# Optimization experiments

Hardware: AMD Instinct MI355X
Metric: run time of the kernel (lower is better)

## Reference

```python
import jax, jax.numpy as jnp
import numpy as np

B, T, Rn, D, O, E, H, C, TM = 20, 20, 20, 4096, 16, 512, 8, 68, 1900


def l2norm(x, axis=-1, eps=1e-12):
    return x / jnp.maximum(jnp.linalg.norm(x, axis=axis, keepdims=True), eps)


def setup_inputs() -> dict:
    key = jax.random.key(0)
    ks = jax.random.split(key, 10)
    return {
        "features": jax.random.normal(ks[0], (B, T, Rn, D), jnp.float32),
        "labels": jax.random.randint(ks[1], (B, O), 0, C),
        "temporal_mem": jax.random.normal(ks[2], (TM, T, D), jnp.float32),
        "entity_W": jax.random.normal(ks[3], (C, E), jnp.float32) / np.float32(np.sqrt(C)),
        "entity_b": jnp.zeros((E,), jnp.float32),
        "Wq": jax.random.normal(ks[4], (E, E), jnp.float32) / np.float32(np.sqrt(E)),
        "Wk": jax.random.normal(ks[5], (D, E), jnp.float32) / np.float32(np.sqrt(D)),
        "Wv": jax.random.normal(ks[6], (D, E), jnp.float32) / np.float32(np.sqrt(D)),
        "Wo": jax.random.normal(ks[7], (E, E), jnp.float32) / np.float32(np.sqrt(E)),
        "obj_W1": jax.random.normal(ks[8], (D, E), jnp.float32) / np.float32(np.sqrt(D)),
        "obj_b1": jnp.zeros((E,), jnp.float32),
        "obj_W2": jax.random.normal(ks[9], (E, 1), jnp.float32) / np.float32(np.sqrt(E)),
        "obj_b2": jnp.zeros((1,), jnp.float32),
    }


def reference(features, labels, temporal_mem, entity_W, entity_b, Wq, Wk, Wv, Wo,
              obj_W1, obj_b1, obj_W2, obj_b2):
    beta = 0.5   # loss mixing weight (module's beta)
    qgce = 0.7   # generalized-CE exponent
    Dh = E // H
    # region features, L2-normalized (dataset_feat == 'CVPR' path)
    Rf = l2norm(features)                                   # [B,T,Rn,D]

    # ---- temporal memory-bank kNN retrieval ----
    R_max = l2norm(jnp.max(Rf, axis=2))                     # [B,T,D] max-pool over regions
    mem_max = l2norm(jnp.max(temporal_mem, axis=1))         # [TM,D] max-pool over frames
    sim = jnp.einsum('btd,md->btm', R_max, mem_max)         # [B,T,TM]
    idx = jnp.argmax(sim, axis=-1)                          # [B,T] nearest memory slot
    Rp = temporal_mem[idx]                                  # [B,T,T,D] gathered memory videos
    mem_feat = jnp.max(Rp, axis=2)                          # [B,T,D]

    # ---- entity (object-label) embedding: one-hot with class 0 zeroed ----
    onehot = jax.nn.one_hot(labels, C, dtype=features.dtype)
    onehot = onehot * (labels != 0)[..., None].astype(features.dtype)
    Qe = onehot @ entity_W + entity_b                       # [B,O,E]

    # ---- multi-head attention fusion over regions + retrieved memory ----
    kv = jnp.concatenate([Rf.reshape(B, T * Rn, D), mem_feat], axis=1)  # [B,N,D]
    q = (Qe @ Wq).reshape(B, O, H, Dh)
    k = (kv @ Wk).reshape(B, -1, H, Dh)
    v = (kv @ Wv).reshape(B, -1, H, Dh)
    scores = jnp.einsum('bohd,bnhd->bhon', q, k) / np.float32(np.sqrt(Dh))
    attn = jax.nn.softmax(scores, axis=-1)
    fused = jnp.einsum('bhon,bnhd->bohd', attn, v).reshape(B, O, E) @ Wo  # [B,O,E]

    # ---- top-k region objectness selection + generalized CE ----
    QR = jax.lax.stop_gradient(jnp.mean(scores, axis=1)[:, :, :T * Rn].reshape(B, O, T, Rn))
    hi = jnp.argmax(QR, axis=-1)                            # [B,O,T] top-1 region
    lo = jnp.argmin(QR, axis=-1)                            # [B,O,T] low region
    bidx = jnp.arange(B)[:, None, None]
    tidx = jnp.arange(T)[None, None, :]
    R_high = Rf[bidx, tidx, hi]                             # [B,O,T,D]
    R_low = Rf[bidx, tidx, lo]                              # [B,O,T,D]
    osel = (labels != 0).astype(features.dtype)             # [B,O]
    onum = jnp.maximum(jnp.sum(osel, axis=1), 1.0)
    mlp = lambda x: jax.nn.sigmoid(jnp.tanh(x @ obj_W1 + obj_b1) @ obj_W2 + obj_b2)
    s_hi = mlp(R_high * osel[..., None, None]).squeeze(-1)  # [B,O,T]
    s_lo = mlp(R_low * osel[..., None, None]).squeeze(-1)
    gce_hi = jnp.mean((1.0 - (s_hi + 1e-7) ** qgce) / qgce * osel[..., None], axis=-1)
    gce_lo = jnp.mean((1.0 - (1.0 - s_lo + 1e-7) ** qgce) / qgce * osel[..., None], axis=-1)
    gce = jnp.mean(jnp.sum(gce_hi, axis=1) / onum) + jnp.mean(jnp.sum(gce_lo, axis=1) / onum)

    return fused + beta * gce
```

## Files before the change

### kernel.cpp

```cpp
#include <hip/hip_runtime.h>

#define B_   20
#define T_   20
#define RN   20
#define D_   4096
#define O_   16
#define E_   512
#define H_   8
#define DH   64
#define TM_  1900
#define NKV  420
#define MROWS (B_*NKV)
#define MPAD 8448
#define NW   1536
#define NSIM 1920
#define MSIM 512
#define CAP  256
#define SIMK 8

using f32x4  = __attribute__((ext_vector_type(4))) float;
using bf16x8 = __attribute__((ext_vector_type(8))) __bf16;

__device__ __forceinline__ unsigned short f2bf(float f){
  unsigned u = __float_as_uint(f);
  u += 0x7fffu + ((u >> 16) & 1u);
  return (unsigned short)(u >> 16);
}

__device__ __forceinline__ void st_bf4(unsigned short* dst, float4 v){
  ushort4 o = make_ushort4(f2bf(v.x), f2bf(v.y), f2bf(v.z), f2bf(v.w));
  *(ushort4*)dst = o;
}

__device__ __forceinline__ float bsum256(float v, float* sh){
  int t = threadIdx.x;
  for (int o = 32; o; o >>= 1) v += __shfl_down(v, o, 64);
  __syncthreads();
  if ((t & 63) == 0) sh[t >> 6] = v;
  __syncthreads();
  return sh[0] + sh[1] + sh[2] + sh[3];
}

__device__ __forceinline__ float bmax256(float v, float* sh){
  int t = threadIdx.x;
  for (int o = 32; o; o >>= 1) v = fmaxf(v, __shfl_down(v, o, 64));
  __syncthreads();
  if ((t & 63) == 0) sh[t >> 6] = v;
  __syncthreads();
  return fmaxf(fmaxf(sh[0], sh[1]), fmaxf(sh[2], sh[3]));
}

__device__ __forceinline__ void gld16(const void* g, void* l){
  __builtin_amdgcn_global_load_lds(
      (const __attribute__((address_space(1))) unsigned int*)g,
      (__attribute__((address_space(3))) unsigned int*)l, 16, 0, 0);
}

__global__ __launch_bounds__(256) void k_pre(
    const float* __restrict__ F, const float* __restrict__ TMm,
    const float* __restrict__ Wk, const float* __restrict__ Wv, const float* __restrict__ W1,
    unsigned short* __restrict__ Wall,
    unsigned short* __restrict__ A, float* __restrict__ rmaxr, float* __restrict__ rmsum,
    unsigned short* __restrict__ ubf,
    float* __restrict__ umax, float* __restrict__ msum, unsigned short* __restrict__ wnorm,
    const int* __restrict__ labels, const float* __restrict__ entW, const float* __restrict__ entB,
    const float* __restrict__ Wq, float* __restrict__ q){
  __shared__ char smem[4352];
  int bid = blockIdx.x, t = threadIdx.x;
  if (bid < 1920){
    int m = bid;
    if (m >= TM_){
      int4 zz = make_int4(0,0,0,0);
      int4* row = (int4*)(wnorm + (size_t)m*D_);
      row[t] = zz; row[t + 256] = zz;
      return;
    }
    float* sh = (float*)smem;
    const float* base = TMm + (size_t)m*T_*D_;
    float4 mx[4];
#pragma unroll
    for (int i = 0; i < 4; ++i) mx[i] = make_float4(-1e30f,-1e30f,-1e30f,-1e30f);
    for (int f = 0; f < T_; ++f){
#pragma unroll
      for (int i = 0; i < 4; ++i){
        float4 v = *(const float4*)(base + (size_t)f*D_ + i*1024 + t*4);
        mx[i].x = fmaxf(mx[i].x, v.x); mx[i].y = fmaxf(mx[i].y, v.y);
        mx[i].z = fmaxf(mx[i].z, v.z); mx[i].w = fmaxf(mx[i].w, v.w);
      }
    }
    float s = 0.f;
#pragma unroll
    for (int i = 0; i < 4; ++i){
      *(float4*)(umax + (size_t)m*D_ + i*1024 + t*4) = mx[i];
      s += mx[i].x*mx[i].x + mx[i].y*mx[i].y + mx[i].z*mx[i].z + mx[i].w*mx[i].w;
    }
    s = bsum256(s, sh);
    if (t == 0) msum[m] = s;
    float inv = 1.f / fmaxf(sqrtf(s), 1e-12f);
#pragma unroll
    for (int i = 0; i < 4; ++i){
      float4 u = mx[i];
      u.x *= inv; u.y *= inv; u.z *= inv; u.w *= inv;
      st_bf4(wnorm + (size_t)m*D_ + i*1024 + t*4, u);
    }
  } else if (bid < 2432){
    int bt = bid - 1920;
    if (bt >= 400){
      int4 zz = make_int4(0,0,0,0);
      int4* row = (int4*)(ubf + (size_t)bt*D_);
      row[t] = zz; row[t + 256] = zz;
      return;
    }
    float* sh = (float*)smem;
    int b = bt / T_, tt = bt % T_;
    const float* fb = F + (size_t)bt*RN*D_;
    unsigned short* ab = A + ((size_t)b*NKV + (size_t)tt*RN)*D_;
    float4 mx[4];
#pragma unroll
    for (int i = 0; i < 4; ++i) mx[i] = make_float4(-1e30f,-1e30f,-1e30f,-1e30f);
    for (int r = 0; r < RN; ++r){
      float4 v[4];
      float s = 0.f;
#pragma unroll
      for (int i = 0; i < 4; ++i){
        v[i] = *(const float4*)(fb + (size_t)r*D_ + i*1024 + t*4);
        s += v[i].x*v[i].x + v[i].y*v[i].y + v[i].z*v[i].z + v[i].w*v[i].w;
      }
      s = bsum256(s, sh);
      float ri = 1.f / fmaxf(sqrtf(s), 1e-12f);
#pragma unroll
      for (int i = 0; i < 4; ++i){
        v[i].x *= ri; v[i].y *= ri; v[i].z *= ri; v[i].w *= ri;
        st_bf4(ab + (size_t)r*D_ + i*1024 + t*4, v[i]);
        mx[i].x = fmaxf(mx[i].x, v[i].x); mx[i].y = fmaxf(mx[i].y, v[i].y);
        mx[i].z = fmaxf(mx[i].z, v[i].z); mx[i].w = fmaxf(mx[i].w, v[i].w);
      }
    }
    float s2 = 0.f;
#pragma unroll
    for (int i = 0; i < 4; ++i){
      *(float4*)(rmaxr + (size_t)bt*D_ + i*1024 + t*4) = mx[i];
      s2 += mx[i].x*mx[i].x + mx[i].y*mx[i].y + mx[i].z*mx[i].z + mx[i].w*mx[i].w;
    }
    s2 = bsum256(s2, sh);
    if (t == 0) rmsum[bt] = s2;
    float inv = 1.f / fmaxf(sqrtf(s2), 1e-12f);
#pragma unroll
    for (int i = 0; i < 4; ++i){
      float4 u = mx[i];
      u.x *= inv; u.y *= inv; u.z *= inv; u.w *= inv;
      st_bf4(ubf + (size_t)bt*D_ + i*1024 + t*4, u);
    }
  } else if (bid < 8576){
    int wti = bid - 2432;
    float* tile = (float*)smem;
    int kb = (wti & 127) * 32, nb = (wti >> 7) * 32;
    const float* src; int nc0;
    if (nb < 512)      { src = Wk; nc0 = nb; }
    else if (nb < 1024){ src = Wv; nc0 = nb - 512; }
    else               { src = W1; nc0 = nb - 1024; }
    int tx = t & 31, ty = t >> 5;
#pragma unroll
    for (int j = 0; j < 4; ++j){
      int k = kb + ty + j*8;
      tile[(ty + j*8)*33 + tx] = src[(size_t)k*E_ + nc0 + tx];
    }
    __syncthreads();
#pragma unroll
    for (int j = 0; j < 4; ++j){
      int n = nb + ty + j*8;
      int k = kb + tx;
      Wall[(size_t)n*D_ + k] = f2bf(tile[tx*33 + ty + j*8]);
    }
  } else {
    int bo = bid - 8576;
    float* qe = (float*)smem;
    int lab = labels[bo];
    float sel = (lab != 0) ? 1.f : 0.f;
    qe[t]       = sel * entW[(size_t)lab*E_ + t]       + entB[t];
    qe[t + 256] = sel * entW[(size_t)lab*E_ + t + 256] + entB[t + 256];
    __syncthreads();
    float a0 = 0.f, a1 = 0.f;
    for (int ep = 0; ep < E_; ++ep){
      float r = qe[ep];
      a0 += r * Wq[(size_t)ep*E_ + t];
      a1 += r * Wq[(size_t)ep*E_ + t + 256];
    }
    q[(size_t)bo*E_ + t] = a0;
    q[(size_t)bo*E_ + t + 256] = a1;
  }
}

__global__ __launch_bounds__(256, 2) void k_gemm(const unsigned short* __restrict__ A,
                                                 const unsigned short* __restrict__ Bw,
                                                 float* __restrict__ C,
                                                 int nNt, int ldc, int doswz, int nwg,
                                                 int nblk, int nkt, size_t cpart){
  __shared__ char lds[32768];
  int part = blockIdx.x / nblk;
  int bid  = blockIdx.x % nblk;
  if (doswz){ int q = nwg >> 3; bid = (bid & 7)*q + (bid >> 3); }
  int mt = bid / nNt, nt = bid % nNt;
  int tid = threadIdx.x, wv = tid >> 6, l = tid & 63;
  int wr = (wv >> 1) * 64, wc = (wv & 1) * 64;
  const char* Ab = (const char*)A + (size_t)mt*128*(size_t)(D_*2);
  const char* Bb = (const char*)Bw + (size_t)nt*128*(size_t)(D_*2);
  C += (size_t)part * cpart;
  f32x4 acc[4][4];
#pragma unroll
  for (int m = 0; m < 4; ++m)
#pragma unroll
    for (int n = 0; n < 4; ++n) acc[m][n] = (f32x4){0.f,0.f,0.f,0.f};
  int kt0 = part * nkt;
  for (int kt = kt0; kt < kt0 + nkt; ++kt){
    int ktoff = kt*128;
#pragma unroll
    for (int i = 0; i < 4; ++i){
      int idx = i*256 + tid;
      int row = idx >> 3, u = idx & 7;
      int ul = u ^ (row & 7);
      gld16(Ab + (size_t)row*(D_*2) + ktoff + ul*16, lds + i*4096 + wv*1024);
      gld16(Bb + (size_t)row*(D_*2) + ktoff + ul*16, lds + 16384 + i*4096 + wv*1024);
    }
    __syncthreads();
#pragma unroll
    for (int kk = 0; kk < 2; ++kk){
      bf16x8 av[4], bv[4];
#pragma unroll
      for (int m = 0; m < 4; ++m){
        int row = wr + m*16 + (l & 15);
        int u = (kk*4 + (l >> 4)) ^ (row & 7);
        av[m] = *(const bf16x8*)(lds + row*128 + u*16);
      }
#pragma unroll
      for (int n = 0; n < 4; ++n){
        int row = wc + n*16 + (l & 15);
        int u = (kk*4 + (l >> 4)) ^ (row & 7);
        bv[n] = *(const bf16x8*)(lds + 16384 + row*128 + u*16);
      }
#pragma unroll
      for (int m = 0; m < 4; ++m)
#pragma unroll
        for (int n = 0; n < 4; ++n)
          acc[m][n] = __builtin_amdgcn_mfma_f32_16x16x32_bf16(av[m], bv[n], acc[m][n], 0, 0, 0);
    }
    __syncthreads();
  }
  int rq = (l >> 4) * 4, cq = l & 15;
  size_t crow0 = (size_t)mt*128 + wr, ccol0 = (size_t)nt*128 + wc;
#pragma unroll
  for (int m = 0; m < 4; ++m)
#pragma unroll
    for (int n = 0; n < 4; ++n){
      size_t r0 = crow0 + m*16 + rq, c0 = ccol0 + n*16 + cq;
#pragma unroll
      for (int j = 0; j < 4; ++j)
        C[(r0 + j)*ldc + c0] = acc[m][n][j];
    }
}

__global__ __launch_bounds__(512, 1) void k_gemm256(const unsigned short* __restrict__ A,
                                                    const unsigned short* __restrict__ Bw,
                                                    float* __restrict__ C,
                                                    int nNt, int ldc, int nwg){
  __shared__ char lds[131072];
  int bid = blockIdx.x;
  {
    int q8 = nwg >> 3, r8 = nwg & 7, x = bid & 7, s = bid >> 3;
    bid = (x < r8 ? x*(q8+1) : r8*(q8+1) + (x-r8)*q8) + s;
  }
  int mt = bid / nNt, nt = bid % nNt;
  int tid = threadIdx.x, wid = tid >> 6, l = tid & 63;
  int wr = (wid >> 2) * 128;
  int wc = (wid & 3) * 64;
  int fr = l & 15, fq = l >> 4;
  const char* Ab = (const char*)A + (size_t)mt*256*(size_t)(D_*2);
  const char* Bb = (const char*)Bw + (size_t)nt*256*(size_t)(D_*2);
  f32x4 acc[8][4];
#pragma unroll
  for (int m = 0; m < 8; ++m)
#pragma unroll
    for (int n = 0; n < 4; ++n) acc[m][n] = (f32x4){0.f,0.f,0.f,0.f};

#pragma unroll
  for (int i = 0; i < 4; ++i){
    int idx = i*512 + tid;
    int row = idx >> 3, u = idx & 7;
    int ul = u ^ (row & 7);
    gld16(Ab + (size_t)row*(D_*2) + (size_t)(ul*16), lds + idx*16);
    gld16(Bb + (size_t)row*(D_*2) + (size_t)(ul*16), lds + 32768 + idx*16);
  }
  __syncthreads();

  int c = 0;
  for (int kt = 0; kt < D_/64; ++kt){
    if (kt < D_/64 - 1){
      int ktoff = (kt + 1) * 128;
      char* dA = lds + (c^1)*65536;
      char* dB = dA + 32768;
#pragma unroll
      for (int i = 0; i < 4; ++i){
        int idx = i*512 + tid;
        int row = idx >> 3, u = idx & 7;
        int ul = u ^ (row & 7);
        gld16(Ab + (size_t)row*(D_*2) + ktoff + ul*16, dA + idx*16);
        gld16(Bb + (size_t)row*(D_*2) + ktoff + ul*16, dB + idx*16);
      }
    }
    const char* LA = lds + c*65536;
    const char* LB = LA + 32768;
    bf16x8 bv[4][2];
#pragma unroll
    for (int n = 0; n < 4; ++n)
#pragma unroll
      for (int kk = 0; kk < 2; ++kk){
        int row = wc + n*16 + fr;
        int u = (kk*4 + fq) ^ (row & 7);
        bv[n][kk] = *(const bf16x8*)(LB + row*128 + u*16);
      }
    __builtin_amdgcn_s_setprio(1);
#pragma unroll
    for (int mp = 0; mp < 4; ++mp){
      bf16x8 av[2][2];
#pragma unroll
      for (int mm = 0; mm < 2; ++mm)
#pragma unroll
        for (int kk = 0; kk < 2; ++kk){
          int row = wr + (mp*2 + mm)*16 + fr;
          int u = (kk*4 + fq) ^ (row & 7);
          av[mm][kk] = *(const bf16x8*)(LA + row*128 + u*16);
        }
#pragma unroll
      for (int mm = 0; mm < 2; ++mm)
#pragma unroll
        for (int n = 0; n < 4; ++n)
#pragma unroll
          for (int kk = 0; kk < 2; ++kk)
            acc[mp*2 + mm][n] = __builtin_amdgcn_mfma_f32_16x16x32_bf16(
                av[mm][kk], bv[n][kk], acc[mp*2 + mm][n], 0, 0, 0);
    }
    __builtin_amdgcn_s_setprio(0);
    __syncthreads();
    c ^= 1;
  }
  size_t crow0 = (size_t)mt*256 + wr, ccol0 = (size_t)nt*256 + wc;
#pragma unroll
  for (int m = 0; m < 8; ++m)
#pragma unroll
    for (int n = 0; n < 4; ++n){
      size_t r0 = crow0 + m*16 + fq*4, c0 = ccol0 + n*16 + fr;
#pragma unroll
      for (int j = 0; j < 4; ++j)
        C[(r0 + j)*ldc + c0] = acc[m][n][j];
    }
}

__global__ __launch_bounds__(256) void k_pick(const float* __restrict__ simp,
                                              const float* __restrict__ rmaxr, const float* __restrict__ rmsum,
                                              const float* __restrict__ umax, const float* __restrict__ msum,
                                              unsigned short* __restrict__ A){
  int bt = blockIdx.x, t = threadIdx.x;
  if (bt >= 400){
    int4 z = make_int4(0,0,0,0);
    int4* row = (int4*)(A + (size_t)(MROWS + bt - 400)*D_);
    row[t] = z; row[t + 256] = z;
    return;
  }
  __shared__ float srow[NSIM];
  __shared__ float sh[4];
  __shared__ int cnt;
  __shared__ int cl[CAP];
  for (int m = t; m < NSIM; m += 256){
    float s = 0.f;
#pragma unroll
    for (int p = 0; p < SIMK; ++p)
      s += simp[(size_t)p*MSIM*NSIM + (size_t)bt*NSIM + m];
    srow[m] = s;
  }
  if (t == 0) cnt = 0;
  __syncthreads();
  float mx = -1e30f;
  for (int m = t; m < TM_; m += 256) mx = fmaxf(mx, srow[m]);
  mx = bmax256(mx, sh);
  float thr = mx - 2.5e-4f;
  for (int m = t; m < TM_; m += 256){
    if (srow[m] >= thr){
      int p = atomicAdd(&cnt, 1);
      if (p < CAP) cl[p] = m;
    }
  }
  __syncthreads();
  int cn = cnt < CAP ? cnt : CAP;
  float rinvv = 1.f / fmaxf(sqrtf(rmsum[bt]), 1e-12f);
  const float* a = rmaxr + (size_t)bt*D_;
  float best = -1e30f; int bestm = 0x7fffffff;
  for (int ci = 0; ci < cn; ++ci){
    int m = cl[ci];
    const float* wrow = umax + (size_t)m*D_;
    float p = 0.f;
    for (int i = t*4; i < D_; i += 1024){
      float4 av = *(const float4*)(a + i);
      float4 wv = *(const float4*)(wrow + i);
      p += av.x*wv.x + av.y*wv.y + av.z*wv.z + av.w*wv.w;
    }
    p = bsum256(p, sh);
    float sim = p * rinvv * (1.f / fmaxf(sqrtf(msum[m]), 1e-12f));
    if (sim > best || (sim == best && m < bestm)){ best = sim; bestm = m; }
  }
  int b = bt / T_, tt = bt % T_;
  unsigned short* dst = A + ((size_t)b*NKV + 400 + tt)*D_;
  const float* src = umax + (size_t)bestm*D_;
#pragma unroll
  for (int i = 0; i < 4; ++i){
    size_t off = (size_t)i*1024 + t*4;
    float4 v = *(const float4*)(src + off);
    st_bf4(dst + off, v);
  }
}

__global__ __launch_bounds__(256) void k_post(const float* __restrict__ q, const float* __restrict__ c2,
                                              float* __restrict__ fpre, int* __restrict__ hi,
                                              int* __restrict__ lo, const float* __restrict__ b1,
                                              const float* __restrict__ W2, const float* __restrict__ b2,
                                              float* __restrict__ z){
  __shared__ char smem[58368];
  int bid = blockIdx.x, t = threadIdx.x;
  if (bid < 160){
    int b = bid >> 3, h = bid & 7;
    int w = t >> 6, l = t & 63;
    float* qhp = (float*)smem;
    float* kb  = (float*)(smem + 4160);
    float* sc  = (float*)(smem + 31460);
    for (int i = t; i < O_*DH; i += 256){
      int o = i >> 6, d = i & 63;
      qhp[o*65 + d] = q[((size_t)(b*O_ + o))*E_ + h*DH + d] * 0.125f;
    }
    __syncthreads();
    for (int c = 0; c < 4; ++c){
      for (int i = t; i < 105*DH; i += 256){
        int j = i >> 6, d = i & 63;
        kb[j*65 + d] = c2[((size_t)(b*NKV + c*105 + j))*NW + h*DH + d];
      }
      __syncthreads();
      for (int i = t; i < O_*105; i += 256){
        int o = i / 105, j = i % 105;
        float acc = 0.f;
        for (int d = 0; d < DH; ++d) acc += qhp[o*65 + d] * kb[j*65 + d];
        sc[o*420 + c*105 + j] = acc;
      }
      __syncthreads();
    }
    for (int oi = 0; oi < 4; ++oi){
      int o = w + oi*4;
      float mx = -1e30f;
      for (int n = l; n < NKV; n += 64) mx = fmaxf(mx, sc[o*420 + n]);
      for (int of = 32; of; of >>= 1) mx = fmaxf(mx, __shfl_xor(mx, of, 64));
      float sum = 0.f;
      for (int n = l; n < NKV; n += 64){ float e = expf(sc[o*420 + n] - mx); sc[o*420 + n] = e; sum += e; }
      for (int of = 32; of; of >>= 1) sum += __shfl_xor(sum, of, 64);
      float inv = 1.f / sum;
      for (int n = l; n < NKV; n += 64) sc[o*420 + n] *= inv;
    }
    __syncthreads();
    float acc[4] = {0.f, 0.f, 0.f, 0.f};
    for (int c = 0; c < 4; ++c){
      for (int i = t; i < 105*DH; i += 256){
        int j = i >> 6, d = i & 63;
        kb[j*65 + d] = c2[((size_t)(b*NKV + c*105 + j))*NW + E_ + h*DH + d];
      }
      __syncthreads();
#pragma unroll
      for (int og = 0; og < 4; ++og){
        int o = og*4 + w;
        float a = 0.f;
        for (int j = 0; j < 105; ++j) a += sc[o*420 + c*105 + j] * kb[j*65 + l];
        acc[og] += a;
      }
      __syncthreads();
    }
#pragma unroll
    for (int og = 0; og < 4; ++og){
      int o = og*4 + w;
      fpre[((size_t)(b*O_ + o))*E_ + h*DH + l] = acc[og];
    }
  } else if (bid < 560){
    int bt = bid - 160;
    int b = bt / T_, tt = bt % T_;
    float* kl = (float*)smem;
    float* qr = (float*)(smem + 41040);
    for (int i = t; i < RN*E_; i += 256){
      int r = i >> 9, e = i & 511;
      kl[r*513 + e] = c2[((size_t)(b*NKV + tt*RN + r))*NW + e];
    }
    __syncthreads();
#pragma unroll
    for (int pp = 0; pp < 2; ++pp){
      int p = t + pp*256;
      if (p < O_*RN){
        int o = p / RN, r = p % RN;
        const float* qrow = q + ((size_t)(b*O_ + o))*E_;
        float acc = 0.f;
        for (int e = 0; e < E_; ++e) acc += qrow[e] * kl[r*513 + e];
        qr[o*20 + r] = acc;
      }
    }
    __syncthreads();
    if (t < O_){
      int o = t;
      float bh = qr[o*20], bl = qr[o*20]; int ih = 0, il = 0;
#pragma unroll
      for (int r = 1; r < RN; ++r){
        float v = qr[o*20 + r];
        if (v > bh){ bh = v; ih = r; }
        if (v < bl){ bl = v; il = r; }
      }
      int rowbase = b*NKV + tt*RN;
      int outi = (b*O_ + o)*T_ + tt;
      hi[outi] = rowbase + ih;
      lo[outi] = rowbase + il;
    }
  } else {
    int g = (bid - 560)*4 + (t >> 6);
    int l = t & 63;
    int b = g / 400, j = g % 400;
    int row = b*NKV + j;
    const float* hrow = c2 + (size_t)row*NW + 1024;
    float acc = 0.f;
    for (int e = l; e < E_; e += 64) acc += tanhf(hrow[e] + b1[e]) * W2[e];
    for (int of = 32; of; of >>= 1) acc += __shfl_down(acc, of, 64);
    if (l == 0) z[row] = 1.f / (1.f + expf(-(acc + b2[0])));
  }
}

__global__ __launch_bounds__(256) void k_outg(const float* __restrict__ fpre, const float* __restrict__ Wo,
                                              const float* __restrict__ z, const int* __restrict__ hi,
                                              const int* __restrict__ lo, const int* __restrict__ labels,
                                              float* __restrict__ out){
  int bo = blockIdx.x, t = threadIdx.x;
  __shared__ float rowv[E_];
  __shared__ float vb[B_];
  __shared__ int cb[B_];
  __shared__ float gsh;
  rowv[t] = fpre[(size_t)bo*E_ + t];
  rowv[t + 256] = fpre[(size_t)bo*E_ + t + 256];
  if (t < B_){ vb[t] = 0.f; cb[t] = 0; }
  __syncthreads();
  for (int p = t; p < B_*O_; p += 256){
    int b = p / O_;
    if (labels[p] != 0){
      float acc = 0.f;
      for (int tt = 0; tt < T_; ++tt){
        float shi = z[hi[p*T_ + tt]];
        float slo = z[lo[p*T_ + tt]];
        acc += (1.f - __powf(shi + 1e-7f, 0.7f)) / 0.7f;
        acc += (1.f - __powf(1.f - slo + 1e-7f, 0.7f)) / 0.7f;
      }
      atomicAdd(&vb[b], acc / (float)T_);
      atomicAdd(&cb[b], 1);
    }
  }
  __syncthreads();
  if (t == 0){
    float g = 0.f;
    for (int b = 0; b < B_; ++b) g += vb[b] / fmaxf((float)cb[b], 1.f);
    gsh = 0.5f * (g / (float)B_);
  }
  __syncthreads();
  float g = gsh;
  float a0 = 0.f, a1 = 0.f;
  for (int ep = 0; ep < E_; ++ep){
    float r = rowv[ep];
    a0 += r * Wo[(size_t)ep*E_ + t];
    a1 += r * Wo[(size_t)ep*E_ + t + 256];
  }
  out[(size_t)bo*E_ + t] = a0 + g;
  out[(size_t)bo*E_ + t + 256] = a1 + g;
}

extern "C" void kernel_launch(void* const* d_in, const int* in_sizes, int n_in,
                              void* d_out, int out_size, void* d_ws, size_t ws_size,
                              hipStream_t stream) {
  (void)in_sizes; (void)n_in; (void)out_size; (void)ws_size;
  const float* F    = (const float*)d_in[0];
  const int*   labels = (const int*)d_in[1];
  const float* TMm  = (const float*)d_in[2];
  const float* entW = (const float*)d_in[3];
  const float* entB = (const float*)d_in[4];
  const float* Wq   = (const float*)d_in[5];
  const float* Wk   = (const float*)d_in[6];
  const float* Wv   = (const float*)d_in[7];
  const float* Wo   = (const float*)d_in[8];
  const float* W1   = (const float*)d_in[9];
  const float* b1   = (const float*)d_in[10];
  const float* W2   = (const float*)d_in[11];
  const float* b2   = (const float*)d_in[12];
  float* out = (float*)d_out;

  size_t off = 0;
  char* wsb = (char*)d_ws;
  auto alloc = [&](size_t bytes) -> char* {
    char* p = wsb + off; off += (bytes + 255) & ~(size_t)255; return p;
  };
  unsigned short* A_kv = (unsigned short*)alloc((size_t)MPAD * D_ * 2);
  unsigned short* Wall = (unsigned short*)alloc((size_t)NW * D_ * 2);
  float* umax          = (float*)alloc((size_t)TM_ * D_ * 4);
  char*  c2reg         = alloc((size_t)MPAD * NW * 4);
  float* C2    = (float*)c2reg;
  unsigned short* wnorm = (unsigned short*)c2reg;
  float* simp  = (float*)(c2reg + 15728640);
  unsigned short* ubf = (unsigned short*)alloc((size_t)MSIM * D_ * 2);
  float* rmaxr = (float*)alloc((size_t)400 * D_ * 4);
  float* qbuf  = (float*)alloc((size_t)B_ * O_ * E_ * 4);
  float* fpre  = (float*)alloc((size_t)B_ * O_ * E_ * 4);
  float* rmsum = (float*)alloc(400 * 4);
  float* msum  = (float*)alloc(TM_ * 4);
  int*   hib   = (int*)alloc(6400 * 4);
  int*   lob   = (int*)alloc(6400 * 4);
  float* zbuf  = (float*)alloc((size_t)MROWS * 4);

  k_pre<<<8896, 256, 0, stream>>>(F, TMm, Wk, Wv, W1, Wall, A_kv, rmaxr, rmsum, ubf,
                                  umax, msum, wnorm, labels, entW, entB, Wq, qbuf);
  k_gemm<<<(MSIM/128)*(NSIM/128)*SIMK, 256, 0, stream>>>(ubf, wnorm, simp, NSIM/128, NSIM, 0, 60,
                                                         (MSIM/128)*(NSIM/128), (D_/64)/SIMK,
                                                         (size_t)MSIM*NSIM);
  k_pick<<<448, 256, 0, stream>>>(simp, rmaxr, rmsum, umax, msum, A_kv);
  k_gemm256<<<(MPAD/256)*(NW/256), 512, 0, stream>>>(A_kv, Wall, C2, NW/256, NW,
                                                     (MPAD/256)*(NW/256));
  k_post<<<2560, 256, 0, stream>>>(qbuf, C2, fpre, hib, lob, b1, W2, b2, zbuf);
  k_outg<<<B_*O_, 256, 0, stream>>>(fpre, Wo, zbuf, hib, lob, labels, out);
}
```

Measured before the change: 501.9 us.

## Precompute projections of all memory slots and fuse three GEMMs into one launch

Instead of gathering the chosen memory slot's max-pooled features into the KV activation matrix and projecting them after kNN selection, every memory slot's max-pooled vector is projected through Wk/Wv/W1 up front. The similarity GEMM, the region GEMM and the memory GEMM now run as one 256-workgroup launch. k_pick then only copies one projected row, which removes the serial dependency of the big GEMM on the argmax and drops the split-K similarity pass. The cost is extra GEMM work over 2048 memory rows and some extra buffers. It also adds a one-row register prefetch of the next region in the feature normalization loop.

```diff
diff --git a/kernel.cpp b/kernel.cpp
--- a/kernel.cpp
+++ b/kernel.cpp
@@ -9,14 +9,11 @@
 #define H_   8
 #define DH   64
 #define TM_  1900
-#define NKV  420
-#define MROWS (B_*NKV)
-#define MPAD 8448
+#define MREG 8192
 #define NW   1536
-#define NSIM 1920
+#define NSIM 2048
 #define MSIM 512
 #define CAP  256
-#define SIMK 8
 
 using f32x4  = __attribute__((ext_vector_type(4))) float;
 using bf16x8 = __attribute__((ext_vector_type(8))) __bf16;
@@ -63,16 +60,19 @@
     unsigned short* __restrict__ A, float* __restrict__ rmaxr, float* __restrict__ rmsum,
     unsigned short* __restrict__ ubf,
     float* __restrict__ umax, float* __restrict__ msum, unsigned short* __restrict__ wnorm,
+    unsigned short* __restrict__ gbf,
     const int* __restrict__ labels, const float* __restrict__ entW, const float* __restrict__ entB,
     const float* __restrict__ Wq, float* __restrict__ q){
   __shared__ char smem[4352];
   int bid = blockIdx.x, t = threadIdx.x;
-  if (bid < 1920){
+  if (bid < 2048){
     int m = bid;
     if (m >= TM_){
       int4 zz = make_int4(0,0,0,0);
-      int4* row = (int4*)(wnorm + (size_t)m*D_);
-      row[t] = zz; row[t + 256] = zz;
+      int4* r1 = (int4*)(wnorm + (size_t)m*D_);
+      int4* r2 = (int4*)(gbf + (size_t)m*D_);
+      r1[t] = zz; r1[t + 256] = zz;
+      r2[t] = zz; r2[t + 256] = zz;
       return;
     }
     float* sh = (float*)smem;
@@ -92,6 +92,7 @@
 #pragma unroll
     for (int i = 0; i < 4; ++i){
       *(float4*)(umax + (size_t)m*D_ + i*1024 + t*4) = mx[i];
+      st_bf4(gbf + (size_t)m*D_ + i*1024 + t*4, mx[i]);
       s += mx[i].x*mx[i].x + mx[i].y*mx[i].y + mx[i].z*mx[i].z + mx[i].w*mx[i].w;
     }
     s = bsum256(s, sh);
@@ -103,28 +104,43 @@
       u.x *= inv; u.y *= inv; u.z *= inv; u.w *= inv;
       st_bf4(wnorm + (size_t)m*D_ + i*1024 + t*4, u);
     }
-  } else if (bid < 2432){
-    int bt = bid - 1920;
+  } else if (bid < 2560){
+    int bt = bid - 2048;
     if (bt >= 400){
       int4 zz = make_int4(0,0,0,0);
-      int4* row = (int4*)(ubf + (size_t)bt*D_);
-      row[t] = zz; row[t + 256] = zz;
+      int4* r1 = (int4*)(ubf + (size_t)bt*D_);
+      r1[t] = zz; r1[t + 256] = zz;
+      int base = 8000 + (bt - 400)*2;
+#pragma unroll
+      for (int k = 0; k < 2; ++k){
+        if (base + k < MREG){
+          int4* r2 = (int4*)(A + (size_t)(base + k)*D_);
+          r2[t] = zz; r2[t + 256] = zz;
+        }
+      }
       return;
     }
     float* sh = (float*)smem;
-    int b = bt / T_, tt = bt % T_;
     const float* fb = F + (size_t)bt*RN*D_;
-    unsigned short* ab = A + ((size_t)b*NKV + (size_t)tt*RN)*D_;
+    unsigned short* ab = A + (size_t)bt*RN*D_;
     float4 mx[4];
 #pragma unroll
     for (int i = 0; i < 4; ++i) mx[i] = make_float4(-1e30f,-1e30f,-1e30f,-1e30f);
+    float4 vn[4];
+#pragma unroll
+    for (int i = 0; i < 4; ++i) vn[i] = *(const float4*)(fb + i*1024 + t*4);
     for (int r = 0; r < RN; ++r){
       float4 v[4];
       float s = 0.f;
 #pragma unroll
       for (int i = 0; i < 4; ++i){
-        v[i] = *(const float4*)(fb + (size_t)r*D_ + i*1024 + t*4);
+        v[i] = vn[i];
         s += v[i].x*v[i].x + v[i].y*v[i].y + v[i].z*v[i].z + v[i].w*v[i].w;
+      }
+      if (r + 1 < RN){
+#pragma unroll
+        for (int i = 0; i < 4; ++i)
+          vn[i] = *(const float4*)(fb + (size_t)(r+1)*D_ + i*1024 + t*4);
       }
       s = bsum256(s, sh);
       float ri = 1.f / fmaxf(sqrtf(s), 1e-12f);
@@ -151,8 +167,8 @@
       u.x *= inv; u.y *= inv; u.z *= inv; u.w *= inv;
       st_bf4(ubf + (size_t)bt*D_ + i*1024 + t*4, u);
     }
-  } else if (bid < 8576){
-    int wti = bid - 2432;
+  } else if (bid < 8704){
+    int wti = bid - 2560;
     float* tile = (float*)smem;
     int kb = (wti & 127) * 32, nb = (wti >> 7) * 32;
     const float* src; int nc0;
@@ -173,7 +189,7 @@
       Wall[(size_t)n*D_ + k] = f2bf(tile[tx*33 + ty + j*8]);
     }
   } else {
-    int bo = bid - 8576;
+    int bo = bid - 8704;
     float* qe = (float*)smem;
     int lab = labels[bo];
     float sel = (lab != 0) ? 1.f : 0.f;
@@ -191,85 +207,20 @@
   }
 }
 
-__global__ __launch_bounds__(256, 2) void k_gemm(const unsigned short* __restrict__ A,
-                                                 const unsigned short* __restrict__ Bw,
-                                                 float* __restrict__ C,
-                                                 int nNt, int ldc, int doswz, int nwg,
-                                                 int nblk, int nkt, size_t cpart){
-  __shared__ char lds[32768];
-  int part = blockIdx.x / nblk;
-  int bid  = blockIdx.x % nblk;
-  if (doswz){ int q = nwg >> 3; bid = (bid & 7)*q + (bid >> 3); }
-  int mt = bid / nNt, nt = bid % nNt;
-  int tid = threadIdx.x, wv = tid >> 6, l = tid & 63;
-  int wr = (wv >> 1) * 64, wc = (wv & 1) * 64;
-  const char* Ab = (const char*)A + (size_t)mt*128*(size_t)(D_*2);
-  const char* Bb = (const char*)Bw + (size_t)nt*128*(size_t)(D_*2);
-  C += (size_t)part * cpart;
-  f32x4 acc[4][4];
-#pragma unroll
-  for (int m = 0; m < 4; ++m)
-#pragma unroll
-    for (int n = 0; n < 4; ++n) acc[m][n] = (f32x4){0.f,0.f,0.f,0.f};
-  int kt0 = part * nkt;
-  for (int kt = kt0; kt < kt0 + nkt; ++kt){
-    int ktoff = kt*128;
-#pragma unroll
-    for (int i = 0; i < 4; ++i){
-      int idx = i*256 + tid;
-      int row = idx >> 3, u = idx & 7;
-      int ul = u ^ (row & 7);
-      gld16(Ab + (size_t)row*(D_*2) + ktoff + ul*16, lds + i*4096 + wv*1024);
-      gld16(Bb + (size_t)row*(D_*2) + ktoff + ul*16, lds + 16384 + i*4096 + wv*1024);
-    }
-    __syncthreads();
-#pragma unroll
-    for (int kk = 0; kk < 2; ++kk){
-      bf16x8 av[4], bv[4];
-#pragma unroll
-      for (int m = 0; m < 4; ++m){
-        int row = wr + m*16 + (l & 15);
-        int u = (kk*4 + (l >> 4)) ^ (row & 7);
-        av[m] = *(const bf16x8*)(lds + row*128 + u*16);
-      }
-#pragma unroll
-      for (int n = 0; n < 4; ++n){
-        int row = wc + n*16 + (l & 15);
-        int u = (kk*4 + (l >> 4)) ^ (row & 7);
-        bv[n] = *(const bf16x8*)(lds + 16384 + row*128 + u*16);
-      }
-#pragma unroll
-      for (int m = 0; m < 4; ++m)
-#pragma unroll
-        for (int n = 0; n < 4; ++n)
-          acc[m][n] = __builtin_amdgcn_mfma_f32_16x16x32_bf16(av[m], bv[n], acc[m][n], 0, 0, 0);
-    }
-    __syncthreads();
-  }
-  int rq = (l >> 4) * 4, cq = l & 15;
-  size_t crow0 = (size_t)mt*128 + wr, ccol0 = (size_t)nt*128 + wc;
-#pragma unroll
-  for (int m = 0; m < 4; ++m)
-#pragma unroll
-    for (int n = 0; n < 4; ++n){
-      size_t r0 = crow0 + m*16 + rq, c0 = ccol0 + n*16 + cq;
-#pragma unroll
-      for (int j = 0; j < 4; ++j)
-        C[(r0 + j)*ldc + c0] = acc[m][n][j];
-    }
-}
-
-__global__ __launch_bounds__(512, 1) void k_gemm256(const unsigned short* __restrict__ A,
-                                                    const unsigned short* __restrict__ Bw,
-                                                    float* __restrict__ C,
-                                                    int nNt, int ldc, int nwg){
+__global__ __launch_bounds__(512, 1) void k_gemm3(
+    const unsigned short* __restrict__ Akv, const unsigned short* __restrict__ Wall,
+    const unsigned short* __restrict__ ubf, const unsigned short* __restrict__ wnorm,
+    const unsigned short* __restrict__ gbf,
+    float* __restrict__ C2, float* __restrict__ simc, float* __restrict__ Gc){
   __shared__ char lds[131072];
   int bid = blockIdx.x;
-  {
-    int q8 = nwg >> 3, r8 = nwg & 7, x = bid & 7, s = bid >> 3;
-    bid = (x < r8 ? x*(q8+1) : r8*(q8+1) + (x-r8)*q8) + s;
-  }
-  int mt = bid / nNt, nt = bid % nNt;
+  bid = (bid & 7)*32 + (bid >> 3);
+  const unsigned short *A, *Bw; float* C; int nNt, ldc, mt, nt;
+  if (bid < 192){       A = Akv; Bw = Wall;  C = C2;   nNt = 6; ldc = NW;   mt = bid/6;  nt = bid%6; }
+  else if (bid < 208){  int s = bid - 192;
+                        A = ubf; Bw = wnorm; C = simc; nNt = 8; ldc = NSIM; mt = s/8;    nt = s%8; }
+  else {                int s = bid - 208;
+                        A = gbf; Bw = Wall;  C = Gc;   nNt = 6; ldc = NW;   mt = s/6;    nt = s%6; }
   int tid = threadIdx.x, wid = tid >> 6, l = tid & 63;
   int wr = (wid >> 2) * 128;
   int wc = (wid & 3) * 64;
@@ -351,32 +302,20 @@
       size_t r0 = crow0 + m*16 + fq*4, c0 = ccol0 + n*16 + fr;
 #pragma unroll
       for (int j = 0; j < 4; ++j)
-        C[(r0 + j)*ldc + c0] = acc[m][n][j];
-    }
-}
-
-__global__ __launch_bounds__(256) void k_pick(const float* __restrict__ simp,
+        C[(r0 + j)*(size_t)ldc + c0] = acc[m][n][j];
+    }
+}
+
+__global__ __launch_bounds__(256) void k_pick(const float* __restrict__ simc,
                                               const float* __restrict__ rmaxr, const float* __restrict__ rmsum,
                                               const float* __restrict__ umax, const float* __restrict__ msum,
-                                              unsigned short* __restrict__ A){
+                                              const float* __restrict__ Gc, float* __restrict__ C2){
   int bt = blockIdx.x, t = threadIdx.x;
-  if (bt >= 400){
-    int4 z = make_int4(0,0,0,0);
-    int4* row = (int4*)(A + (size_t)(MROWS + bt - 400)*D_);
-    row[t] = z; row[t + 256] = z;
-    return;
-  }
-  __shared__ float srow[NSIM];
+  __shared__ float srow[1920];
   __shared__ float sh[4];
   __shared__ int cnt;
   __shared__ int cl[CAP];
-  for (int m = t; m < NSIM; m += 256){
-    float s = 0.f;
-#pragma unroll
-    for (int p = 0; p < SIMK; ++p)
-      s += simp[(size_t)p*MSIM*NSIM + (size_t)bt*NSIM + m];
-    srow[m] = s;
-  }
+  for (int m = t; m < TM_; m += 256) srow[m] = simc[(size_t)bt*NSIM + m];
   if (t == 0) cnt = 0;
   __syncthreads();
   float mx = -1e30f;
@@ -407,15 +346,9 @@
     float sim = p * rinvv * (1.f / fmaxf(sqrtf(msum[m]), 1e-12f));
     if (sim > best || (sim == best && m < bestm)){ best = sim; bestm = m; }
   }
-  int b = bt / T_, tt = bt % T_;
-  unsigned short* dst = A + ((size_t)b*NKV + 400 + tt)*D_;
-  const float* src = umax + (size_t)bestm*D_;
-#pragma unroll
-  for (int i = 0; i < 4; ++i){
-    size_t off = (size_t)i*1024 + t*4;
-    float4 v = *(const float4*)(src + off);
-    st_bf4(dst + off, v);
-  }
+  const float4* src = (const float4*)(Gc + (size_t)bestm*NW);
+  float4* dst = (float4*)(C2 + (size_t)(MREG + bt)*NW);
+  if (t < 128){ dst[t] = src[t]; dst[t + 128] = src[t + 128]; dst[t + 256] = src[t + 256]; }
 }
 
 __global__ __launch_bounds__(256) void k_post(const float* __restrict__ q, const float* __restrict__ c2,
@@ -439,7 +372,9 @@
     for (int c = 0; c < 4; ++c){
       for (int i = t; i < 105*DH; i += 256){
         int j = i >> 6, d = i & 63;
-        kb[j*65 + d] = c2[((size_t)(b*NKV + c*105 + j))*NW + h*DH + d];
+        int n = c*105 + j;
+        size_t row = n < 400 ? (size_t)b*400 + n : (size_t)MREG + b*20 + (n - 400);
+        kb[j*65 + d] = c2[row*NW + h*DH + d];
       }
       __syncthreads();
       for (int i = t; i < O_*105; i += 256){
@@ -452,21 +387,23 @@
     }
     for (int oi = 0; oi < 4; ++oi){
       int o = w + oi*4;
-      float mx = -1e30f;
-      for (int n = l; n < NKV; n += 64) mx = fmaxf(mx, sc[o*420 + n]);
-      for (int of = 32; of; of >>= 1) mx = fmaxf(mx, __shfl_xor(mx, of, 64));
+      float mxv = -1e30f;
+      for (int n = l; n < 420; n += 64) mxv = fmaxf(mxv, sc[o*420 + n]);
+      for (int of = 32; of; of >>= 1) mxv = fmaxf(mxv, __shfl_xor(mxv, of, 64));
       float sum = 0.f;
-      for (int n = l; n < NKV; n += 64){ float e = expf(sc[o*420 + n] - mx); sc[o*420 + n] = e; sum += e; }
+      for (int n = l; n < 420; n += 64){ float e = expf(sc[o*420 + n] - mxv); sc[o*420 + n] = e; sum += e; }
       for (int of = 32; of; of >>= 1) sum += __shfl_xor(sum, of, 64);
       float inv = 1.f / sum;
-      for (int n = l; n < NKV; n += 64) sc[o*420 + n] *= inv;
+      for (int n = l; n < 420; n += 64) sc[o*420 + n] *= inv;
     }
     __syncthreads();
     float acc[4] = {0.f, 0.f, 0.f, 0.f};
     for (int c = 0; c < 4; ++c){
       for (int i = t; i < 105*DH; i += 256){
         int j = i >> 6, d = i & 63;
-        kb[j*65 + d] = c2[((size_t)(b*NKV + c*105 + j))*NW + E_ + h*DH + d];
+        int n = c*105 + j;
+        size_t row = n < 400 ? (size_t)b*400 + n : (size_t)MREG + b*20 + (n - 400);
+        kb[j*65 + d] = c2[row*NW + E_ + h*DH + d];
       }
       __syncthreads();
 #pragma unroll
@@ -490,7 +427,7 @@
     float* qr = (float*)(smem + 41040);
     for (int i = t; i < RN*E_; i += 256){
       int r = i >> 9, e = i & 511;
-      kl[r*513 + e] = c2[((size_t)(b*NKV + tt*RN + r))*NW + e];
+      kl[r*513 + e] = c2[((size_t)b*400 + tt*RN + r)*NW + e];
     }
     __syncthreads();
 #pragma unroll
@@ -514,7 +451,7 @@
         if (v > bh){ bh = v; ih = r; }
         if (v < bl){ bl = v; il = r; }
       }
-      int rowbase = b*NKV + tt*RN;
+      int rowbase = b*400 + tt*RN;
       int outi = (b*O_ + o)*T_ + tt;
       hi[outi] = rowbase + ih;
       lo[outi] = rowbase + il;
@@ -522,13 +459,11 @@
   } else {
     int g = (bid - 560)*4 + (t >> 6);
     int l = t & 63;
-    int b = g / 400, j = g % 400;
-    int row = b*NKV + j;
-    const float* hrow = c2 + (size_t)row*NW + 1024;
+    const float* hrow = c2 + (size_t)g*NW + 1024;
     float acc = 0.f;
     for (int e = l; e < E_; e += 64) acc += tanhf(hrow[e] + b1[e]) * W2[e];
     for (int of = 32; of; of >>= 1) acc += __shfl_down(acc, of, 64);
-    if (l == 0) z[row] = 1.f / (1.f + expf(-(acc + b2[0])));
+    if (l == 0) z[g] = 1.f / (1.f + expf(-(acc + b2[0])));
   }
 }
 
@@ -601,31 +536,28 @@
   auto alloc = [&](size_t bytes) -> char* {
     char* p = wsb + off; off += (bytes + 255) & ~(size_t)255; return p;
   };
-  unsigned short* A_kv = (unsigned short*)alloc((size_t)MPAD * D_ * 2);
+  unsigned short* A_kv = (unsigned short*)alloc((size_t)MREG * D_ * 2);
   unsigned short* Wall = (unsigned short*)alloc((size_t)NW * D_ * 2);
   float* umax          = (float*)alloc((size_t)TM_ * D_ * 4);
-  char*  c2reg         = alloc((size_t)MPAD * NW * 4);
-  float* C2    = (float*)c2reg;
-  unsigned short* wnorm = (unsigned short*)c2reg;
-  float* simp  = (float*)(c2reg + 15728640);
-  unsigned short* ubf = (unsigned short*)alloc((size_t)MSIM * D_ * 2);
+  unsigned short* gbf  = (unsigned short*)alloc((size_t)NSIM * D_ * 2);
+  unsigned short* wnorm= (unsigned short*)alloc((size_t)NSIM * D_ * 2);
+  unsigned short* ubf  = (unsigned short*)alloc((size_t)MSIM * D_ * 2);
   float* rmaxr = (float*)alloc((size_t)400 * D_ * 4);
+  float* simc  = (float*)alloc((size_t)MSIM * NSIM * 4);
+  float* Gc    = (float*)alloc((size_t)NSIM * NW * 4);
+  float* C2    = (float*)alloc((size_t)(MREG + 512) * NW * 4);
   float* qbuf  = (float*)alloc((size_t)B_ * O_ * E_ * 4);
   float* fpre  = (float*)alloc((size_t)B_ * O_ * E_ * 4);
   float* rmsum = (float*)alloc(400 * 4);
   float* msum  = (float*)alloc(TM_ * 4);
   int*   hib   = (int*)alloc(6400 * 4);
   int*   lob   = (int*)alloc(6400 * 4);
-  float* zbuf  = (float*)alloc((size_t)MROWS * 4);
-
-  k_pre<<<8896, 256, 0, stream>>>(F, TMm, Wk, Wv, W1, Wall, A_kv, rmaxr, rmsum, ubf,
-                                  umax, msum, wnorm, labels, entW, entB, Wq, qbuf);
-  k_gemm<<<(MSIM/128)*(NSIM/128)*SIMK, 256, 0, stream>>>(ubf, wnorm, simp, NSIM/128, NSIM, 0, 60,
-                                                         (MSIM/128)*(NSIM/128), (D_/64)/SIMK,
-                                                         (size_t)MSIM*NSIM);
-  k_pick<<<448, 256, 0, stream>>>(simp, rmaxr, rmsum, umax, msum, A_kv);
-  k_gemm256<<<(MPAD/256)*(NW/256), 512, 0, stream>>>(A_kv, Wall, C2, NW/256, NW,
-                                                     (MPAD/256)*(NW/256));
+  float* zbuf  = (float*)alloc(8000 * 4);
+
+  k_pre<<<9024, 256, 0, stream>>>(F, TMm, Wk, Wv, W1, Wall, A_kv, rmaxr, rmsum, ubf,
+                                  umax, msum, wnorm, gbf, labels, entW, entB, Wq, qbuf);
+  k_gemm3<<<256, 512, 0, stream>>>(A_kv, Wall, ubf, wnorm, gbf, C2, simc, Gc);
+  k_pick<<<400, 256, 0, stream>>>(simc, rmaxr, rmsum, umax, msum, Gc, C2);
   k_post<<<2560, 256, 0, stream>>>(qbuf, C2, fpre, hib, lob, b1, W2, b2, zbuf);
   k_outg<<<B_*O_, 256, 0, stream>>>(fpre, Wo, zbuf, hib, lob, labels, out);
 }
```

Result: faster. 485.9 us (-3.2%).
